# Optimization experiments

Hardware: AMD Instinct MI355X
Metric: run time of the kernel (lower is better)

## Reference

```python
import jax, jax.numpy as jnp
import numpy as np
from jax import lax

B, T, S = 8, 512, 512
E, H, V = 512, 1024, 32000
K, L, ML = 3, 6, 1024
PAD_IDX = 1  # padding value used to fill conv left-padding (module quirk: fills with trg_pad_idx)


def setup_inputs() -> dict:
    key = jax.random.key(0)
    ks = jax.random.split(key, 20)
    s = 0.02
    return {
        "trg": jax.random.randint(ks[0], (B, T), 0, V),
        "encoder_conved": jax.random.normal(ks[1], (B, S, E), jnp.float32),
        "encoder_combined": jax.random.normal(ks[2], (B, S, E), jnp.float32),
        "tok_emb": jax.random.normal(ks[3], (V, E), jnp.float32) * s,
        "pos_emb": jax.random.normal(ks[4], (ML, E), jnp.float32) * s,
        "emb2hid_w": jax.random.normal(ks[5], (E, H), jnp.float32) * s,
        "emb2hid_b": jnp.zeros((H,), jnp.float32),
        "hid2emb_w": jax.random.normal(ks[6], (H, E), jnp.float32) * s,
        "hid2emb_b": jnp.zeros((E,), jnp.float32),
        "attn_hid2emb_w": jax.random.normal(ks[7], (H, E), jnp.float32) * s,
        "attn_hid2emb_b": jnp.zeros((E,), jnp.float32),
        "attn_emb2hid_w": jax.random.normal(ks[8], (E, H), jnp.float32) * s,
        "attn_emb2hid_b": jnp.zeros((H,), jnp.float32),
        "fc_out_w": jax.random.normal(ks[9], (E, V), jnp.float32) * s,
        "fc_out_b": jnp.zeros((V,), jnp.float32),
        "conv_w": jax.random.normal(ks[10], (L, 2 * H, H, K), jnp.float32) * s,
        "conv_b": jnp.zeros((L, 2 * H), jnp.float32),
    }


def reference(trg, encoder_conved, encoder_combined, tok_emb, pos_emb,
              emb2hid_w, emb2hid_b, hid2emb_w, hid2emb_b,
              attn_hid2emb_w, attn_hid2emb_b, attn_emb2hid_w, attn_emb2hid_b,
              fc_out_w, fc_out_b, conv_w, conv_b):
    scale = jnp.sqrt(jnp.float32(0.5))
    # embeddings: (B, T, E)
    embedded = tok_emb[trg] + pos_emb[jnp.arange(T)][None, :, :]
    # emb -> hid, move to channels-first: (B, H, T)
    conv_input = jnp.transpose(embedded @ emb2hid_w + emb2hid_b, (0, 2, 1))

    pad = jnp.full((B, H, K - 1), jnp.float32(PAD_IDX))
    dn = lax.conv_dimension_numbers((B, H, T + K - 1), (2 * H, H, K), ('NCH', 'OIH', 'NCH'))

    for l in range(L):
        padded = jnp.concatenate([pad, conv_input], axis=2)  # (B, H, T+K-1)
        conved = lax.conv_general_dilated(padded, conv_w[l], (1,), 'VALID',
                                          dimension_numbers=dn)
        conved = conved + conv_b[l][None, :, None]  # (B, 2H, T)
        a, g = jnp.split(conved, 2, axis=1)
        conved = a * jax.nn.sigmoid(g)  # GLU -> (B, H, T)
        # attention
        conved_emb = jnp.transpose(conved, (0, 2, 1)) @ attn_hid2emb_w + attn_hid2emb_b  # (B,T,E)
        combined = (conved_emb + embedded) * scale
        energy = jnp.einsum('bte,bse->bts', combined, encoder_conved)
        attention = jax.nn.softmax(energy, axis=2)
        attended = jnp.einsum('bts,bse->bte', attention, encoder_combined)
        attended = attended @ attn_emb2hid_w + attn_emb2hid_b  # (B,T,H)
        conved = (conved + jnp.transpose(attended, (0, 2, 1))) * scale
        conv_input = (conved + conv_input) * scale

    conv_output = jnp.transpose(conv_input, (0, 2, 1)) @ hid2emb_w + hid2emb_b  # (B,T,E)
    pred_output = conv_output @ fc_out_w + fc_out_b  # (B,T,V)
    return pred_output
```

## Files before the change

kernel.cpp:

```cpp
#include <hip/hip_runtime.h>

typedef __bf16 bf16_t;
typedef __bf16 bf16x8 __attribute__((ext_vector_type(8)));
typedef float f32x4 __attribute__((ext_vector_type(4)));

#define SQH 0.70710678118654752440f

__device__ __forceinline__ void gld_lds16(const bf16_t* g, bf16_t* l) {
  __builtin_amdgcn_global_load_lds(
      (__attribute__((address_space(1))) void*)(void*)(g),
      (__attribute__((address_space(3))) void*)(l), 16, 0, 0);
}

template<int MODE>
__global__ __launch_bounds__(256, 2)
void k_gemm_nt(const bf16_t* __restrict__ A, const bf16_t* __restrict__ B,
               const float* __restrict__ bias,
               float* __restrict__ Cf, bf16_t* __restrict__ Cb,
               const float* __restrict__ aux0, float* __restrict__ aux1,
               int K, int lda, int ldb, int ldc, int ldcb,
               int pad2, int bshift, int seglog2, int clog2,
               int cbpad2, int cbshift,
               long long saB, long long sbB, long long scB)
{
  __shared__ __align__(16) bf16_t sA[128 * 32];
  __shared__ __align__(16) bf16_t sB[128 * 32];

  const int tid  = threadIdx.x;
  const int wave = tid >> 6;
  const int lane = tid & 63;
  const int z    = blockIdx.z;
  A += (long long)z * saB;
  B += (long long)z * sbB;
  if (Cf) Cf += (long long)z * scB;
  if (Cb) Cb += (long long)z * scB;

  const int m0 = blockIdx.y * 128;
  const int n0 = blockIdx.x * 128;

  const int rq = tid >> 2;
  const int qo = (tid & 3) * 8;

  bf16_t* lA0 = sA + wave * 512;
  bf16_t* lA1 = sA + 2048 + wave * 512;
  bf16_t* lB0 = sB + wave * 512;
  bf16_t* lB1 = sB + 2048 + wave * 512;

  const int wm = (wave & 1) * 64;
  const int wn = (wave >> 1) * 64;
  const int lm = lane & 15;
  const int lk = (lane >> 4) * 8;

  f32x4 acc[4][4] = {};
  const int kmask = (1 << seglog2) - 1;

  for (int k0 = 0; k0 < K; k0 += 32) {
    const int kseg = k0 >> seglog2;
    const int kcol = k0 & kmask;
    {
      const int m1 = m0 + rq;
      const int m2 = m1 + 64;
      const long long ar1 = m1 + pad2 * (m1 >> clog2) + bshift + kseg;
      const long long ar2 = m2 + pad2 * (m2 >> clog2) + bshift + kseg;
      gld_lds16(A + ar1 * lda + kcol + qo, lA0);
      gld_lds16(A + ar2 * lda + kcol + qo, lA1);
      const long long nr = n0 + rq;
      gld_lds16(B + nr * ldb + k0 + qo, lB0);
      gld_lds16(B + (nr + 64) * ldb + k0 + qo, lB1);
    }
    __syncthreads();
    bf16x8 af[4], bfr[4];
#pragma unroll
    for (int i = 0; i < 4; ++i)
      af[i] = *(const bf16x8*)(sA + (wm + i * 16 + lm) * 32 + lk);
#pragma unroll
    for (int j = 0; j < 4; ++j)
      bfr[j] = *(const bf16x8*)(sB + (wn + j * 16 + lm) * 32 + lk);
#pragma unroll
    for (int i = 0; i < 4; ++i)
#pragma unroll
      for (int j = 0; j < 4; ++j)
        acc[i][j] = __builtin_amdgcn_mfma_f32_16x16x32_bf16(af[i], bfr[j], acc[i][j], 0, 0, 0);
    __syncthreads();
  }

  const int lq = (lane >> 4) * 4;
#pragma unroll
  for (int i = 0; i < 4; ++i) {
#pragma unroll
    for (int j = 0; j < 4; ++j) {
      const int col = n0 + wn + j * 16 + lm;
      const float bv = bias ? bias[col] : 0.0f;
#pragma unroll
      for (int r = 0; r < 4; ++r) {
        const int row = m0 + wm + i * 16 + lq + r;
        float v = acc[i][j][r] + bv;
        if constexpr (MODE == 0) {
          if (Cf) Cf[(long long)row * ldc + col] = v;
          if (Cb) {
            const long long brow = row + cbpad2 * (row >> clog2) + cbshift;
            Cb[brow * ldcb + col] = (bf16_t)v;
          }
        } else if constexpr (MODE == 1) {
          float p = __shfl_xor(v, 1);
          if (!(lane & 1)) {
            float res = v * (1.f / (1.f + __expf(-p)));
            const int h = col >> 1;
            Cf[(long long)row * 1024 + h] = res;
            Cb[(long long)row * 1024 + h] = (bf16_t)res;
          }
        } else if constexpr (MODE == 2) {
          float c = (v + aux0[(long long)row * ldc + col]) * SQH;
          Cb[(long long)row * ldcb + col] = (bf16_t)c;
        } else {
          const long long idx = (long long)row * ldc + col;
          float nv = ((aux0[idx] + v) * SQH + aux1[idx]) * SQH;
          aux1[idx] = nv;
          const long long brow = row + cbpad2 * (row >> clog2) + cbshift;
          Cb[brow * ldcb + col] = (bf16_t)nv;
        }
      }
    }
  }
}

__global__ void k_transpose(const float* __restrict__ in, bf16_t* __restrict__ out,
                            int R, int C, long long sIn, long long sOut) {
  __shared__ float tile[32][33];
  const int b = blockIdx.z;
  in  += (long long)b * sIn;
  out += (long long)b * sOut;
  const int c0 = blockIdx.x * 32;
  const int r0 = blockIdx.y * 32;
  const int tx = threadIdx.x;
  for (int i = threadIdx.y; i < 32; i += 8) {
    int r = r0 + i, c = c0 + tx;
    tile[i][tx] = (r < R && c < C) ? in[(long long)r * C + c] : 0.f;
  }
  __syncthreads();
  for (int i = threadIdx.y; i < 32; i += 8) {
    int c = c0 + i, r = r0 + tx;
    if (c < C && r < R) out[(long long)c * R + r] = (bf16_t)tile[tx][i];
  }
}

__global__ void k_convert(const float* __restrict__ in, bf16_t* __restrict__ out, int n) {
  int i = blockIdx.x * 256 + threadIdx.x;
  if (i < n) out[i] = (bf16_t)in[i];
}

__global__ void k_convw(const float* __restrict__ in, bf16_t* __restrict__ out) {
  const long long s = blockIdx.y;
  const int i = blockIdx.x * 256 + threadIdx.x;
  const float* p = in + s * 3072 + (long long)i * 3;
  float w0 = p[0], w1 = p[1], w2 = p[2];
  const int l = (int)(s >> 11);
  const int o = (int)(s & 2047);
  const int onew = (o < 1024) ? (o << 1) : (((o - 1024) << 1) | 1);
  bf16_t* q = out + ((long long)(l << 11) + onew) * 3072;
  q[i] = (bf16_t)w0; q[1024 + i] = (bf16_t)w1; q[2048 + i] = (bf16_t)w2;
}

__global__ void k_convb(const float* __restrict__ in, float* __restrict__ out) {
  const int i = blockIdx.x * 256 + threadIdx.x;
  const int l = i >> 11;
  const int o = i & 2047;
  const int onew = (o < 1024) ? (o << 1) : (((o - 1024) << 1) | 1);
  out[(l << 11) + onew] = in[i];
}

__global__ void k_embed(const int* __restrict__ trg, const float* __restrict__ tok,
                        const float* __restrict__ pos,
                        float* __restrict__ embF, bf16_t* __restrict__ embB) {
  const long long bt = blockIdx.x;
  const int t = (int)(bt & 511);
  const int id = trg[bt];
  const float* tp = tok + (long long)id * 512;
  const float* pp = pos + (long long)t * 512;
  for (int j = threadIdx.x; j < 512; j += 256) {
    float v = tp[j] + pp[j];
    embF[bt * 512 + j] = v;
    embB[bt * 512 + j] = (bf16_t)v;
  }
}

__global__ void k_padinit(bf16_t* __restrict__ Xp) {
  const int i = blockIdx.x * 256 + threadIdx.x;
  const int b = i >> 11;
  const int r = (i >> 10) & 1;
  const int h = i & 1023;
  Xp[((long long)b * 514 + r) * 1024 + h] = (bf16_t)1.0f;
}

__global__ void k_softmax(const float* __restrict__ E, bf16_t* __restrict__ A) {
  __shared__ float red[8];
  const long long m = blockIdx.x;
  const float* row = E + m * 512;
  const int t = threadIdx.x;
  float x0 = row[t], x1 = row[t + 256];
  float mx = fmaxf(x0, x1);
#pragma unroll
  for (int o = 32; o >= 1; o >>= 1) mx = fmaxf(mx, __shfl_xor(mx, o));
  const int w = t >> 6;
  if ((t & 63) == 0) red[w] = mx;
  __syncthreads();
  mx = fmaxf(fmaxf(red[0], red[1]), fmaxf(red[2], red[3]));
  float e0 = __expf(x0 - mx), e1 = __expf(x1 - mx);
  float s = e0 + e1;
#pragma unroll
  for (int o = 32; o >= 1; o >>= 1) s += __shfl_xor(s, o);
  if ((t & 63) == 0) red[4 + w] = s;
  __syncthreads();
  s = red[4] + red[5] + red[6] + red[7];
  float inv = 1.f / s;
  A[m * 512 + t]       = (bf16_t)(e0 * inv);
  A[m * 512 + t + 256] = (bf16_t)(e1 * inv);
}

extern "C" void kernel_launch(void* const* d_in, const int* in_sizes, int n_in,
                              void* d_out, int out_size, void* d_ws, size_t ws_size,
                              hipStream_t stream) {
  (void)in_sizes; (void)n_in; (void)out_size; (void)ws_size;
  const int*   trg    = (const int*)  d_in[0];
  const float* encCv  = (const float*)d_in[1];
  const float* encCb  = (const float*)d_in[2];
  const float* tokE   = (const float*)d_in[3];
  const float* posE   = (const float*)d_in[4];
  const float* e2h_w  = (const float*)d_in[5];
  const float* e2h_b  = (const float*)d_in[6];
  const float* h2e_w  = (const float*)d_in[7];
  const float* h2e_b  = (const float*)d_in[8];
  const float* ah2e_w = (const float*)d_in[9];
  const float* ah2e_b = (const float*)d_in[10];
  const float* ae2h_w = (const float*)d_in[11];
  const float* ae2h_b = (const float*)d_in[12];
  const float* fc_w   = (const float*)d_in[13];
  const float* fc_b   = (const float*)d_in[14];
  const float* convW  = (const float*)d_in[15];
  const float* convB  = (const float*)d_in[16];
  float* out = (float*)d_out;

  char* cur = (char*)d_ws;
  auto alloc = [&](long long bytes) { char* r = cur; cur += (bytes + 255) & ~255LL; return (void*)r; };

  bf16_t* embA    = (bf16_t*)alloc(4096LL * 512 * 2);
  bf16_t* Xpad    = (bf16_t*)alloc(8LL * 514 * 1024 * 2);
  bf16_t* convedB = (bf16_t*)alloc(4096LL * 1024 * 2);
  bf16_t* combB   = (bf16_t*)alloc(4096LL * 512 * 2);
  bf16_t* attnB   = (bf16_t*)alloc(4096LL * 512 * 2);
  bf16_t* attdB   = (bf16_t*)alloc(4096LL * 512 * 2);
  bf16_t* coutB   = (bf16_t*)alloc(4096LL * 512 * 2);
  bf16_t* wT_e2h  = (bf16_t*)alloc(1024LL * 512 * 2);
  bf16_t* wT_ah2e = (bf16_t*)alloc(512LL * 1024 * 2);
  bf16_t* wT_ae2h = (bf16_t*)alloc(1024LL * 512 * 2);
  bf16_t* wT_h2e  = (bf16_t*)alloc(512LL * 1024 * 2);
  bf16_t* wT_fc   = (bf16_t*)alloc(32000LL * 512 * 2);
  bf16_t* encCvB  = (bf16_t*)alloc(8LL * 512 * 512 * 2);
  bf16_t* encTcb  = (bf16_t*)alloc(8LL * 512 * 512 * 2);
  bf16_t* convWT  = (bf16_t*)alloc(6LL * 2048 * 3072 * 2);
  float*  biasI   = (float*)alloc(6LL * 2048 * 4);
  float*  embF    = (float*)alloc(4096LL * 512 * 4);
  float*  Xf      = (float*)alloc(4096LL * 1024 * 4);
  float*  convedF = (float*)alloc(4096LL * 1024 * 4);
  float*  energy  = (float*)alloc(4096LL * 512 * 4);

  const dim3 tb(32, 8);
  k_transpose<<<dim3(32, 16, 1),  tb, 0, stream>>>(e2h_w,  wT_e2h,  512, 1024, 0, 0);
  k_transpose<<<dim3(16, 32, 1),  tb, 0, stream>>>(ah2e_w, wT_ah2e, 1024, 512, 0, 0);
  k_transpose<<<dim3(32, 16, 1),  tb, 0, stream>>>(ae2h_w, wT_ae2h, 512, 1024, 0, 0);
  k_transpose<<<dim3(16, 32, 1),  tb, 0, stream>>>(h2e_w,  wT_h2e,  1024, 512, 0, 0);
  k_transpose<<<dim3(1000, 16, 1),tb, 0, stream>>>(fc_w,   wT_fc,   512, 32000, 0, 0);
  k_transpose<<<dim3(16, 16, 8),  tb, 0, stream>>>(encCb,  encTcb,  512, 512, 512LL * 512, 512LL * 512);
  k_convert<<<8192, 256, 0, stream>>>(encCv, encCvB, 8 * 512 * 512);
  k_convw<<<dim3(4, 12288), 256, 0, stream>>>(convW, convWT);
  k_convb<<<48, 256, 0, stream>>>(convB, biasI);
  k_embed<<<4096, 256, 0, stream>>>(trg, tokE, posE, embF, embA);
  k_padinit<<<64, 256, 0, stream>>>(Xpad);

  auto gemm0 = [&](const bf16_t* A, const bf16_t* B, const float* bias,
                   float* Cf, bf16_t* Cb, int M, int N, int K,
                   int lda, int ldb, int ldc, int ldcb,
                   int pad2, int bshift, int seglog2,
                   int cbpad2, int cbshift,
                   long long saB, long long sbB, long long scB, int Z) {
    dim3 g(N / 128, M / 128, Z);
    k_gemm_nt<0><<<g, 256, 0, stream>>>(A, B, bias, Cf, Cb, nullptr, nullptr,
                                        K, lda, ldb, ldc, ldcb,
                                        pad2, bshift, seglog2, 9, cbpad2, cbshift,
                                        saB, sbB, scB);
  };

  gemm0(embA, wT_e2h, e2h_b, Xf, Xpad, 4096, 1024, 512,
        512, 512, 1024, 1024, 0, 0, 30, 2, 2, 0, 0, 0, 1);

  for (int l = 0; l < 6; ++l) {
    k_gemm_nt<1><<<dim3(16, 32, 1), 256, 0, stream>>>(
        Xpad, convWT + (long long)l * 2048 * 3072, biasI + l * 2048,
        convedF, convedB, nullptr, nullptr,
        3072, 1024, 3072, 1024, 1024, 2, 0, 10, 9, 0, 0, 0, 0, 0);
    k_gemm_nt<2><<<dim3(4, 32, 1), 256, 0, stream>>>(
        convedB, wT_ah2e, ah2e_b, nullptr, combB, embF, nullptr,
        1024, 1024, 1024, 512, 512, 0, 0, 30, 9, 0, 0, 0, 0, 0);
    gemm0(combB, encCvB, nullptr, energy, nullptr, 512, 512, 512,
          512, 512, 512, 0, 0, 0, 30, 0, 0, 512LL * 512, 512LL * 512, 512LL * 512, 8);
    k_softmax<<<4096, 256, 0, stream>>>(energy, attnB);
    gemm0(attnB, encTcb, nullptr, nullptr, attdB, 512, 512, 512,
          512, 512, 512, 512, 0, 0, 30, 0, 0, 512LL * 512, 512LL * 512, 512LL * 512, 8);
    k_gemm_nt<3><<<dim3(8, 32, 1), 256, 0, stream>>>(
        attdB, wT_ae2h, ae2h_b, nullptr, Xpad, convedF, Xf,
        512, 512, 512, 1024, 1024, 0, 0, 30, 9, 2, 2, 0, 0, 0);
  }

  gemm0(Xpad, wT_h2e, h2e_b, nullptr, coutB, 4096, 512, 1024,
        1024, 1024, 512, 512, 2, 2, 30, 0, 0, 0, 0, 0, 1);
  gemm0(coutB, wT_fc, fc_b, out, nullptr, 4096, 32000, 512,
        512, 512, 32000, 0, 0, 0, 30, 0, 0, 0, 0, 0, 1);
}
```

Measured before the change: 2.052 ms.

## Double-buffer LDS tiles in the bf16 GEMM to overlap loads with MFMA

The shared A/B tiles become two ping-pong buffers. The global-to-LDS load for the next K-slice is issued before the MFMAs on the current slice, and one barrier per iteration replaces two. The launch-bounds occupancy hint is also raised from 2 to 3 blocks per CU. The aim is to hide global load latency behind matrix math. In exchange LDS per block doubles and register pressure is tighter, which could cause spills.

```diff
diff --git a/kernel.cpp b/kernel.cpp
--- a/kernel.cpp
+++ b/kernel.cpp
@@ -13,7 +13,7 @@
 }
 
 template<int MODE>
-__global__ __launch_bounds__(256, 2)
+__global__ __launch_bounds__(256, 3)
 void k_gemm_nt(const bf16_t* __restrict__ A, const bf16_t* __restrict__ B,
                const float* __restrict__ bias,
                float* __restrict__ Cf, bf16_t* __restrict__ Cb,
@@ -23,8 +23,8 @@
                int cbpad2, int cbshift,
                long long saB, long long sbB, long long scB)
 {
-  __shared__ __align__(16) bf16_t sA[128 * 32];
-  __shared__ __align__(16) bf16_t sB[128 * 32];
+  __shared__ __align__(16) bf16_t sA[2][128 * 32];
+  __shared__ __align__(16) bf16_t sB[2][128 * 32];
 
   const int tid  = threadIdx.x;
   const int wave = tid >> 6;
@@ -41,11 +41,6 @@
   const int rq = tid >> 2;
   const int qo = (tid & 3) * 8;
 
-  bf16_t* lA0 = sA + wave * 512;
-  bf16_t* lA1 = sA + 2048 + wave * 512;
-  bf16_t* lB0 = sB + wave * 512;
-  bf16_t* lB1 = sB + 2048 + wave * 512;
-
   const int wm = (wave & 1) * 64;
   const int wn = (wave >> 1) * 64;
   const int lm = lane & 15;
@@ -54,34 +49,43 @@
   f32x4 acc[4][4] = {};
   const int kmask = (1 << seglog2) - 1;
 
-  for (int k0 = 0; k0 < K; k0 += 32) {
+  auto stage = [&](int k0, bf16_t* dA, bf16_t* dB) {
     const int kseg = k0 >> seglog2;
     const int kcol = k0 & kmask;
-    {
-      const int m1 = m0 + rq;
-      const int m2 = m1 + 64;
-      const long long ar1 = m1 + pad2 * (m1 >> clog2) + bshift + kseg;
-      const long long ar2 = m2 + pad2 * (m2 >> clog2) + bshift + kseg;
-      gld_lds16(A + ar1 * lda + kcol + qo, lA0);
-      gld_lds16(A + ar2 * lda + kcol + qo, lA1);
-      const long long nr = n0 + rq;
-      gld_lds16(B + nr * ldb + k0 + qo, lB0);
-      gld_lds16(B + (nr + 64) * ldb + k0 + qo, lB1);
-    }
-    __syncthreads();
+    const int m1 = m0 + rq;
+    const int m2 = m1 + 64;
+    const long long ar1 = m1 + pad2 * (m1 >> clog2) + bshift + kseg;
+    const long long ar2 = m2 + pad2 * (m2 >> clog2) + bshift + kseg;
+    gld_lds16(A + ar1 * lda + kcol + qo, dA + wave * 512);
+    gld_lds16(A + ar2 * lda + kcol + qo, dA + 2048 + wave * 512);
+    const long long nr = n0 + rq;
+    gld_lds16(B + nr * ldb + k0 + qo, dB + wave * 512);
+    gld_lds16(B + (nr + 64) * ldb + k0 + qo, dB + 2048 + wave * 512);
+  };
+
+  const int nt = K >> 5;
+  stage(0, sA[0], sB[0]);
+  __syncthreads();
+
+  int cur = 0;
+  for (int t = 0; t < nt; ++t) {
+    if (t + 1 < nt) stage((t + 1) << 5, sA[cur ^ 1], sB[cur ^ 1]);
+    const bf16_t* pA = sA[cur];
+    const bf16_t* pB = sB[cur];
     bf16x8 af[4], bfr[4];
 #pragma unroll
     for (int i = 0; i < 4; ++i)
-      af[i] = *(const bf16x8*)(sA + (wm + i * 16 + lm) * 32 + lk);
+      af[i] = *(const bf16x8*)(pA + (wm + i * 16 + lm) * 32 + lk);
 #pragma unroll
     for (int j = 0; j < 4; ++j)
-      bfr[j] = *(const bf16x8*)(sB + (wn + j * 16 + lm) * 32 + lk);
+      bfr[j] = *(const bf16x8*)(pB + (wn + j * 16 + lm) * 32 + lk);
 #pragma unroll
     for (int i = 0; i < 4; ++i)
 #pragma unroll
       for (int j = 0; j < 4; ++j)
         acc[i][j] = __builtin_amdgcn_mfma_f32_16x16x32_bf16(af[i], bfr[j], acc[i][j], 0, 0, 0);
-    __syncthreads();
+    if (t + 1 < nt) __syncthreads();
+    cur ^= 1;
   }
 
   const int lq = (lane >> 4) * 4;
```

Measured after the change: 2.049 ms. Within noise of the previous version (-0.1%).
